# Performance work log

Hardware: AMD Instinct MI355X
Metric: run time of the kernel (lower is better)

Reference implementation:

```python
import jax, jax.numpy as jnp
import numpy as np

GRID_NUM = 64
DX = 0.015625  # 1/64 -> unit-cube domain
NDIM = 3
EPS_CLIP = 1e-05
EPS_DIV = 1e-07


def setup_inputs() -> dict:
    key = jax.random.key(0)
    k1, k2, k3 = jax.random.split(key, 3)
    L = 1_000_000
    B = 8
    pos = jax.random.uniform(k1, (L, NDIM), dtype=jnp.float32)          # in [0,1) = domain
    prob = jax.random.uniform(k2, (L,), dtype=jnp.float32)
    batch_indices = jax.random.randint(k3, (L,), 0, B, dtype=jnp.int32)
    return {"pos": pos, "prob": prob, "batch_indices": batch_indices, "batch_size": B}


def _p2g_scatter(pos, prob, batch_indices, batch_size):
    """Quadratic B-spline particle-to-grid scatter. Returns (weight, weight*prob) grids,
    each (batch_size, GRID_NUM**3)."""
    G = GRID_NUM
    G3 = G * G * G
    Xp = pos / DX                                  # (L, 3)
    base = Xp.astype(jnp.int32)                    # floor for non-negative coords
    fx = Xp - base.astype(Xp.dtype)                # (L, 3) fractional part
    # quadratic B-spline weights, stacked over the 3 stencil taps: (3, L, 3)
    w = jnp.stack([0.5 * (1.0 - fx) ** 2,
                   0.75 - (fx - 0.5) ** 2,
                   0.5 * fx ** 2])
    bflat = batch_indices.astype(jnp.int32) * G3
    weight_out = jnp.zeros((batch_size * G3,), dtype=pos.dtype)
    weight_prob_out = jnp.zeros((batch_size * G3,), dtype=pos.dtype)
    # static 3x3x3 neighbor stencil (27 offsets)
    for ox in (-1, 0, 1):
        for oy in (-1, 0, 1):
            for oz in (-1, 0, 1):
                weight = w[ox + 1, :, 0] * w[oy + 1, :, 1] * w[oz + 1, :, 2]  # (L,)
                tx = base[:, 0] + ox
                ty = base[:, 1] + oy
                tz = base[:, 2] + oz
                in_box = ((tx >= 0) & (tx < G) & (ty >= 0) & (ty < G)
                          & (tz >= 0) & (tz < G))
                I = (tx * G + ty) * G + tz
                flat = jnp.where(in_box, bflat + I, 0)
                weight = jnp.where(in_box, weight, jnp.zeros_like(weight))
                weight_out = weight_out.at[flat].add(weight)
                weight_prob_out = weight_prob_out.at[flat].add(weight * prob)
    return (weight_out.reshape(batch_size, G3),
            weight_prob_out.reshape(batch_size, G3))


def reference(pos, prob, batch_indices, batch_size):
    # clip_minmax=True default in the original forward
    pos = jnp.clip(pos, EPS_CLIP, DX * GRID_NUM - EPS_CLIP)
    weight_out, weight_prob_out = _p2g_scatter(pos, prob, batch_indices, batch_size)
    return weight_prob_out / (weight_out + EPS_DIV)  # (B, GRID_NUM**3)
```

## Files before the change

kernel.cpp:

```cpp
#include <hip/hip_runtime.h>


namespace {

constexpr int   G         = 64;
constexpr int   G3        = G * G * G;
constexpr int   BIN       = 16;
constexpr int   NBX       = G / BIN;
constexpr int   BINS_PB   = NBX * NBX * NBX;
constexpr int   TILE      = BIN + 2;
constexpr int   TILE3     = TILE * TILE * TILE;
constexpr int   CAP       = 2560;
constexpr int   PPB       = 2048;
constexpr int   NBINS_MAX = 512;
constexpr float EPS_CLIP  = 1e-5f;
constexpr float EPS_DIV   = 1e-7f;
constexpr float INV_DX    = 64.0f;
constexpr float FXS       = 4398046511104.0f;
constexpr float INV_FXS   = 1.0f / FXS;

static_assert((size_t)TILE3 * 8 < 65536, "K2 LDS over 64KB");

__device__ __forceinline__ float clip01(float v) {
    return fminf(fmaxf(v, EPS_CLIP), 1.0f - EPS_CLIP);
}

__device__ __forceinline__ void bspline_w(float f, float* w) {
    w[0] = 0.5f * (1.0f - f) * (1.0f - f);
    w[1] = 0.75f - (f - 0.5f) * (f - 0.5f);
    w[2] = 0.5f * f * f;
}


__global__ void __launch_bounds__(512)
bin_sort_mat(const float* __restrict__ pos,
             const float* __restrict__ prob,
             const int*   __restrict__ bidx,
             int*         __restrict__ cnt,
             float4*      __restrict__ slots,
             int L) {
    __shared__ unsigned int   s_hist[NBINS_MAX];
    __shared__ unsigned int   s_incl[NBINS_MAX];
    __shared__ unsigned int   s_gbase[NBINS_MAX];
    __shared__ unsigned int   s_wtot[8];
    __shared__ float4         s_pay[PPB];
    __shared__ unsigned short s_bin[PPB];

    const int t    = threadIdx.x;
    const int base = blockIdx.x * PPB;
    const int np   = min(PPB, L - base);

    s_hist[t] = 0u;
    __syncthreads();

    float4   pay[PPB / 512];
    int      pbin[PPB / 512];
    unsigned rank[PPB / 512];
#pragma unroll
    for (int k = 0; k < PPB / 512; ++k) {
        int i = base + k * 512 + t;
        pbin[k] = -1;
        if (i < L) {
            float px = clip01(pos[3 * i + 0]);
            float py = clip01(pos[3 * i + 1]);
            float pz = clip01(pos[3 * i + 2]);
            int bx = (int)(px * INV_DX);
            int by = (int)(py * INV_DX);
            int bz = (int)(pz * INV_DX);
            int b  = ((bidx[i] * NBX + (bx >> 4)) * NBX + (by >> 4)) * NBX
                     + (bz >> 4);
            pay[k]  = make_float4(px, py, pz, prob[i]);
            pbin[k] = b;
            rank[k] = atomicAdd(&s_hist[b], 1u);
        }
    }
    __syncthreads();

    const unsigned c  = s_hist[t];
    const unsigned gb = c ? (unsigned)atomicAdd(&cnt[t], (int)c) : 0u;

    unsigned v = c;
#pragma unroll
    for (int d = 1; d < 64; d <<= 1) {
        unsigned o = __shfl_up(v, d, 64);
        if ((t & 63) >= d) v += o;
    }
    if ((t & 63) == 63) s_wtot[t >> 6] = v;
    __syncthreads();
    unsigned off = 0;
#pragma unroll
    for (int w = 0; w < 8; ++w)
        if (w < (t >> 6)) off += s_wtot[w];
    const unsigned incl = v + off;
    s_incl[t]  = incl;
    s_gbase[t] = gb - (incl - c);
    __syncthreads();

#pragma unroll
    for (int k = 0; k < PPB / 512; ++k) {
        if (pbin[k] >= 0) {
            int b = pbin[k];
            unsigned sp = s_incl[b] - s_hist[b] + rank[k];
            s_pay[sp] = pay[k];
            s_bin[sp] = (unsigned short)b;
        }
    }
    __syncthreads();

    for (int j = t; j < np; j += 512) {
        int b = s_bin[j];
        unsigned g = s_gbase[b] + (unsigned)j;
        if (g < CAP) slots[(size_t)b * CAP + g] = s_pay[j];
    }
}


__global__ void __launch_bounds__(512)
accumulate_bins_pass(const float4* __restrict__ slots,
                     const int*    __restrict__ cnt,
                     float*        __restrict__ tiles_w,
                     float*        __restrict__ tiles_wp) {
    __shared__ unsigned long long t_acc[TILE3];
    const int x     = blockIdx.x;
    const int which = (x >> 3) & 1;
    const int bin   = ((x >> 4) << 3) | (x & 7);
    const int tid   = threadIdx.x;

    for (int j = tid; j < TILE3; j += 512) t_acc[j] = 0ull;
    __syncthreads();

    const int n = min(cnt[bin], CAP);
    const int bx0 = ((bin >> 4) & 3) * BIN;
    const int by0 = ((bin >> 2) & 3) * BIN;
    const int bz0 = (bin & 3) * BIN;
    const float4* sbase = slots + (size_t)bin * CAP;

    for (int s = tid; s < n; s += 512) {
        float4 r = sbase[s];
        float xp = r.x * INV_DX;
        float yp = r.y * INV_DX;
        float zp = r.z * INV_DX;
        int bx = (int)xp, by = (int)yp, bz = (int)zp;
        int l0x = bx - bx0, l0y = by - by0, l0z = bz - bz0;
        if (((l0x | l0y | l0z) & ~15) != 0) continue;
        float wx[3], wy[3], wz[3];
        bspline_w(xp - (float)bx, wx);
        bspline_w(yp - (float)by, wy);
        bspline_w(zp - (float)bz, wz);
        float p = which ? r.w : 1.0f;
#pragma unroll
        for (int a = 0; a < 3; ++a) {
            int ix = (l0x + a) * TILE;
#pragma unroll
            for (int cc = 0; cc < 3; ++cc) {
                int ixy = (ix + l0y + cc) * TILE;
                float wxy = wx[a] * wy[cc] * p;
#pragma unroll
                for (int e = 0; e < 3; ++e) {
                    float v = wxy * wz[e];
                    atomicAdd(&t_acc[ixy + l0z + e],
                              (unsigned long long)(v * FXS));
                }
            }
        }
    }
    __syncthreads();

    float* gt = (which ? tiles_wp : tiles_w) + (size_t)bin * TILE3;
    for (int j = tid; j < TILE3; j += 512) {
        gt[j] = (float)t_acc[j] * INV_FXS;
    }
}


__global__ void finalize_tiles(const float* __restrict__ tiles_w,
                               const float* __restrict__ tiles_wp,
                               float*       __restrict__ out,
                               int total) {
    int c = blockIdx.x * blockDim.x + threadIdx.x;
    if (c >= total) return;
    int cz = c & 63, cy = (c >> 6) & 63, cx = (c >> 12) & 63, b = c >> 18;
    int bx = cx >> 4, mx = cx & 15;
    int by = cy >> 4, my = cy & 15;
    int bz = cz >> 4, mz = cz & 15;

    int xb[2], xl[2], nx = 1; xb[0] = bx; xl[0] = mx + 1;
    if (mx == 0 && bx > 0)            { xb[1] = bx - 1; xl[1] = TILE - 1; nx = 2; }
    else if (mx == 15 && bx < NBX - 1){ xb[1] = bx + 1; xl[1] = 0;        nx = 2; }
    int yb[2], yl[2], ny = 1; yb[0] = by; yl[0] = my + 1;
    if (my == 0 && by > 0)            { yb[1] = by - 1; yl[1] = TILE - 1; ny = 2; }
    else if (my == 15 && by < NBX - 1){ yb[1] = by + 1; yl[1] = 0;        ny = 2; }
    int zb[2], zl[2], nz = 1; zb[0] = bz; zl[0] = mz + 1;
    if (mz == 0 && bz > 0)            { zb[1] = bz - 1; zl[1] = TILE - 1; nz = 2; }
    else if (mz == 15 && bz < NBX - 1){ zb[1] = bz + 1; zl[1] = 0;        nz = 2; }

    float w = 0.f, wp = 0.f;
    for (int i = 0; i < nx; ++i)
        for (int j = 0; j < ny; ++j)
            for (int k = 0; k < nz; ++k) {
                int bin = ((b * NBX + xb[i]) * NBX + yb[j]) * NBX + zb[k];
                size_t idx = (size_t)bin * TILE3
                             + (xl[i] * TILE + yl[j]) * TILE + zl[k];
                w  += tiles_w[idx];
                wp += tiles_wp[idx];
            }
    out[c] = wp / (w + EPS_DIV);
}


__global__ void scatter_interleaved(const float* __restrict__ pos,
                                    const float* __restrict__ prob,
                                    const int*   __restrict__ bidx,
                                    float2*      __restrict__ grid,
                                    int L) {
    int i = blockIdx.x * blockDim.x + threadIdx.x;
    if (i >= L) return;
    float xp = clip01(pos[3 * i + 0]) * INV_DX;
    float yp = clip01(pos[3 * i + 1]) * INV_DX;
    float zp = clip01(pos[3 * i + 2]) * INV_DX;
    int bx = (int)xp, by = (int)yp, bz = (int)zp;
    float wx[3], wy[3], wz[3];
    bspline_w(xp - (float)bx, wx);
    bspline_w(yp - (float)by, wy);
    bspline_w(zp - (float)bz, wz);
    float p = prob[i];
    float2* gbase = grid + (size_t)bidx[i] * G3;
#pragma unroll
    for (int a = 0; a < 3; ++a) {
        int tx = bx + a - 1;
        if (tx < 0 || tx >= G) continue;
#pragma unroll
        for (int c = 0; c < 3; ++c) {
            int ty = by + c - 1;
            if (ty < 0 || ty >= G) continue;
            float wxy = wx[a] * wy[c];
            int rowoff = (tx * G + ty) * G;
#pragma unroll
            for (int e = 0; e < 3; ++e) {
                int tz = bz + e - 1;
                if (tz < 0 || tz >= G) continue;
                float w = wxy * wz[e];
                float2* cell = gbase + rowoff + tz;
                atomicAdd(&cell->x, w);
                atomicAdd(&cell->y, w * p);
            }
        }
    }
}

__global__ void finalize_interleaved(const float2* __restrict__ grid,
                                     float* __restrict__ out, int n) {
    int i = blockIdx.x * blockDim.x + threadIdx.x;
    if (i >= n) return;
    float2 c = grid[i];
    out[i] = c.y / (c.x + EPS_DIV);
}

}

extern "C" void kernel_launch(void* const* d_in, const int* in_sizes, int n_in,
                              void* d_out, int out_size, void* d_ws, size_t ws_size,
                              hipStream_t stream) {
    const float* pos  = (const float*)d_in[0];
    const float* prob = (const float*)d_in[1];
    const int*   bidx = (const int*)d_in[2];
    float* out = (float*)d_out;

    const int L = in_sizes[1];
    const int B = out_size / G3;
    const int nbins = B * BINS_PB;

    const int threads = 256;
    const int k1blocks = (L + PPB - 1) / PPB;
    const int pblocks  = (L + threads - 1) / threads;
    const int fblocks  = (out_size + threads - 1) / threads;

    const size_t tilesw_bytes = (size_t)nbins * TILE3 * sizeof(float);
    const size_t slots_bytes  = (size_t)nbins * CAP * sizeof(float4);
    const size_t cnt_bytes    = (size_t)nbins * sizeof(int);
    const size_t need         = 2 * tilesw_bytes + slots_bytes + cnt_bytes;

    if (ws_size >= need && nbins <= NBINS_MAX && (nbins & 7) == 0) {
        float*  tiles_w  = (float*)d_ws;
        float*  tiles_wp = (float*)((char*)d_ws + tilesw_bytes);
        float4* slots    = (float4*)((char*)d_ws + 2 * tilesw_bytes);
        int*    cnt      = (int*)((char*)d_ws + 2 * tilesw_bytes + slots_bytes);

        hipMemsetAsync(cnt, 0, cnt_bytes, stream);
        bin_sort_mat<<<k1blocks, 512, 0, stream>>>(pos, prob, bidx,
                                                   cnt, slots, L);
        accumulate_bins_pass<<<nbins * 2, 512, 0, stream>>>(slots, cnt,
                                                            tiles_w, tiles_wp);
        finalize_tiles<<<fblocks, threads, 0, stream>>>(tiles_w, tiles_wp,
                                                        out, out_size);
    } else if (ws_size >= (size_t)out_size * 2 * sizeof(float)) {
        float2* grid = (float2*)d_ws;
        hipMemsetAsync(d_ws, 0, (size_t)out_size * 2 * sizeof(float), stream);
        scatter_interleaved<<<pblocks, threads, 0, stream>>>(pos, prob, bidx, grid, L);
        finalize_interleaved<<<fblocks, threads, 0, stream>>>(grid, out, out_size);
    }
}
```

Before: 121.4 us.

## Split accumulation blocks by z-halves of the tile instead of by weight/prob channel

Each bin used to get two blocks, one accumulating weight and one accumulating weight*prob, and each block read every particle in the bin. Now the two blocks split the 18-wide z range of the tile into two 9-wide halves and each accumulates both channels. Particles whose stencil misses a block's half are skipped, so most particles are processed by only one block instead of two. The weight and weight*prob tiles are also interleaved as float2, so finalize does one load per neighbour instead of two. The trade-off is per-tap bounds checks and divergence at the half boundary, plus two LDS atomics per tap where there was one.

```diff
diff --git a/kernel.cpp b/kernel.cpp
--- a/kernel.cpp
+++ b/kernel.cpp
@@ -10,6 +10,8 @@
 constexpr int   BINS_PB   = NBX * NBX * NBX;
 constexpr int   TILE      = BIN + 2;
 constexpr int   TILE3     = TILE * TILE * TILE;
+constexpr int   HZ        = 9;
+constexpr int   HSIZE     = TILE * TILE * HZ;
 constexpr int   CAP       = 2560;
 constexpr int   PPB       = 2048;
 constexpr int   NBINS_MAX = 512;
@@ -19,7 +21,7 @@
 constexpr float FXS       = 4398046511104.0f;
 constexpr float INV_FXS   = 1.0f / FXS;
 
-static_assert((size_t)TILE3 * 8 < 65536, "K2 LDS over 64KB");
+static_assert((size_t)HSIZE * 16 < 65536, "K2 LDS over 64KB");
 
 __device__ __forceinline__ float clip01(float v) {
     return fminf(fmaxf(v, EPS_CLIP), 1.0f - EPS_CLIP);
@@ -116,17 +118,18 @@
 
 
 __global__ void __launch_bounds__(512)
-accumulate_bins_pass(const float4* __restrict__ slots,
-                     const int*    __restrict__ cnt,
-                     float*        __restrict__ tiles_w,
-                     float*        __restrict__ tiles_wp) {
-    __shared__ unsigned long long t_acc[TILE3];
+accumulate_bins_zsplit(const float4* __restrict__ slots,
+                       const int*    __restrict__ cnt,
+                       float2*       __restrict__ tiles) {
+    __shared__ unsigned long long t_w[HSIZE];
+    __shared__ unsigned long long t_wp[HSIZE];
     const int x     = blockIdx.x;
-    const int which = (x >> 3) & 1;
+    const int h     = (x >> 3) & 1;
     const int bin   = ((x >> 4) << 3) | (x & 7);
     const int tid   = threadIdx.x;
-
-    for (int j = tid; j < TILE3; j += 512) t_acc[j] = 0ull;
+    const int zbase = HZ * h;
+
+    for (int j = tid; j < HSIZE; j += 512) { t_w[j] = 0ull; t_wp[j] = 0ull; }
     __syncthreads();
 
     const int n = min(cnt[bin], CAP);
@@ -143,39 +146,48 @@
         int bx = (int)xp, by = (int)yp, bz = (int)zp;
         int l0x = bx - bx0, l0y = by - by0, l0z = bz - bz0;
         if (((l0x | l0y | l0z) & ~15) != 0) continue;
+        int zr = l0z - zbase;
+        if (zr + 2 < 0 || zr > 8) continue;
         float wx[3], wy[3], wz[3];
         bspline_w(xp - (float)bx, wx);
         bspline_w(yp - (float)by, wy);
         bspline_w(zp - (float)bz, wz);
-        float p = which ? r.w : 1.0f;
+        wz[0] *= FXS; wz[1] *= FXS; wz[2] *= FXS;
+        float p = r.w;
 #pragma unroll
         for (int a = 0; a < 3; ++a) {
             int ix = (l0x + a) * TILE;
 #pragma unroll
             for (int cc = 0; cc < 3; ++cc) {
-                int ixy = (ix + l0y + cc) * TILE;
-                float wxy = wx[a] * wy[cc] * p;
+                float wxy  = wx[a] * wy[cc];
+                float wxyp = wxy * p;
+                int row = (ix + l0y + cc) * HZ;
 #pragma unroll
                 for (int e = 0; e < 3; ++e) {
-                    float v = wxy * wz[e];
-                    atomicAdd(&t_acc[ixy + l0z + e],
-                              (unsigned long long)(v * FXS));
+                    int tz = zr + e;
+                    if ((unsigned)tz > 8u) continue;
+                    int ci = row + tz;
+                    atomicAdd(&t_w[ci],  (unsigned long long)(wxy  * wz[e]));
+                    atomicAdd(&t_wp[ci], (unsigned long long)(wxyp * wz[e]));
                 }
             }
         }
     }
     __syncthreads();
 
-    float* gt = (which ? tiles_wp : tiles_w) + (size_t)bin * TILE3;
-    for (int j = tid; j < TILE3; j += 512) {
-        gt[j] = (float)t_acc[j] * INV_FXS;
-    }
-}
-
-
-__global__ void finalize_tiles(const float* __restrict__ tiles_w,
-                               const float* __restrict__ tiles_wp,
-                               float*       __restrict__ out,
+    float2* gt = tiles + (size_t)bin * TILE3;
+    for (int j = tid; j < HSIZE; j += 512) {
+        int tz = j % HZ;
+        int tt = j / HZ;
+        gt[tt * TILE + zbase + tz] =
+            make_float2((float)t_w[j]  * INV_FXS,
+                        (float)t_wp[j] * INV_FXS);
+    }
+}
+
+
+__global__ void finalize_tiles(const float2* __restrict__ tiles,
+                               float*        __restrict__ out,
                                int total) {
     int c = blockIdx.x * blockDim.x + threadIdx.x;
     if (c >= total) return;
@@ -199,10 +211,9 @@
         for (int j = 0; j < ny; ++j)
             for (int k = 0; k < nz; ++k) {
                 int bin = ((b * NBX + xb[i]) * NBX + yb[j]) * NBX + zb[k];
-                size_t idx = (size_t)bin * TILE3
-                             + (xl[i] * TILE + yl[j]) * TILE + zl[k];
-                w  += tiles_w[idx];
-                wp += tiles_wp[idx];
+                float2 v = tiles[(size_t)bin * TILE3
+                                 + (xl[i] * TILE + yl[j]) * TILE + zl[k]];
+                w += v.x; wp += v.y;
             }
     out[c] = wp / (w + EPS_DIV);
 }
@@ -275,24 +286,22 @@
     const int pblocks  = (L + threads - 1) / threads;
     const int fblocks  = (out_size + threads - 1) / threads;
 
-    const size_t tilesw_bytes = (size_t)nbins * TILE3 * sizeof(float);
-    const size_t slots_bytes  = (size_t)nbins * CAP * sizeof(float4);
-    const size_t cnt_bytes    = (size_t)nbins * sizeof(int);
-    const size_t need         = 2 * tilesw_bytes + slots_bytes + cnt_bytes;
+    const size_t tiles_bytes = (size_t)nbins * TILE3 * sizeof(float2);
+    const size_t slots_bytes = (size_t)nbins * CAP * sizeof(float4);
+    const size_t cnt_bytes   = (size_t)nbins * sizeof(int);
+    const size_t need        = tiles_bytes + slots_bytes + cnt_bytes;
 
     if (ws_size >= need && nbins <= NBINS_MAX && (nbins & 7) == 0) {
-        float*  tiles_w  = (float*)d_ws;
-        float*  tiles_wp = (float*)((char*)d_ws + tilesw_bytes);
-        float4* slots    = (float4*)((char*)d_ws + 2 * tilesw_bytes);
-        int*    cnt      = (int*)((char*)d_ws + 2 * tilesw_bytes + slots_bytes);
+        float2* tiles = (float2*)d_ws;
+        float4* slots = (float4*)((char*)d_ws + tiles_bytes);
+        int*    cnt   = (int*)((char*)d_ws + tiles_bytes + slots_bytes);
 
         hipMemsetAsync(cnt, 0, cnt_bytes, stream);
         bin_sort_mat<<<k1blocks, 512, 0, stream>>>(pos, prob, bidx,
                                                    cnt, slots, L);
-        accumulate_bins_pass<<<nbins * 2, 512, 0, stream>>>(slots, cnt,
-                                                            tiles_w, tiles_wp);
-        finalize_tiles<<<fblocks, threads, 0, stream>>>(tiles_w, tiles_wp,
-                                                        out, out_size);
+        accumulate_bins_zsplit<<<nbins * 2, 512, 0, stream>>>(slots, cnt,
+                                                              tiles);
+        finalize_tiles<<<fblocks, threads, 0, stream>>>(tiles, out, out_size);
     } else if (ws_size >= (size_t)out_size * 2 * sizeof(float)) {
         float2* grid = (float2*)d_ws;
         hipMemsetAsync(d_ws, 0, (size_t)out_size * 2 * sizeof(float), stream);
```

New measurement: 130.4 us. 1.07x slower.
